# Optimization experiments

Hardware: AMD Instinct MI355X
Metric: run time of the kernel (lower is better)

The kernel has to match this reference:

```python
import jax, jax.numpy as jnp
import numpy as np

N = 50000
E = 800000
F_IN = 128
H = 128
C = 16


def _balanced_conv(x, row, col, W, b, num_nodes):
    # x: [N, in] -> linear -> gather(row) * norm -> scatter-add(col) + bias
    x = x @ W  # [N, out]
    deg = jax.ops.segment_sum(jnp.ones(row.shape[0], x.dtype), col,
                              num_segments=num_nodes)  # includes self-loops -> deg >= 1
    dinv = deg ** -0.5
    norm = dinv[row] * dinv[col]  # [E+N]
    msg = norm[:, None] * x[row]  # gather + scale
    out = jax.ops.segment_sum(msg, col, num_segments=num_nodes)  # scatter-add
    return out + b


def setup_inputs() -> dict:
    key = jax.random.key(0)
    ks = jax.random.split(key, 12)
    x = jax.random.normal(ks[0], (N, F_IN), dtype=jnp.float32)
    edge_index = jax.random.randint(ks[1], (2, E), 0, N, dtype=jnp.int64)
    s = 1.0 / np.sqrt(F_IN)
    sh = 1.0 / np.sqrt(H)
    return {
        "x": x,
        "edge_index": edge_index,
        "importance": jnp.ones((F_IN,), jnp.float32),
        "W1": jax.random.uniform(ks[2], (F_IN, H), jnp.float32, -s, s),
        "b1": jnp.zeros((H,), jnp.float32),
        "W2": jax.random.uniform(ks[3], (H, H), jnp.float32, -sh, sh),
        "b2": jnp.zeros((H,), jnp.float32),
        "W3": jax.random.uniform(ks[4], (H, H), jnp.float32, -sh, sh),
        "b3": jnp.zeros((H,), jnp.float32),
        "lw1": jax.random.uniform(ks[5], (H, H), jnp.float32, -sh, sh),
        "lb1": jax.random.uniform(ks[6], (H,), jnp.float32, -sh, sh),
        "lw2": jax.random.uniform(ks[7], (H, C), jnp.float32, -sh, sh),
        "lb2": jax.random.uniform(ks[8], (C,), jnp.float32, -sh, sh),
    }


def reference(x, edge_index, importance, W1, b1, W2, b2, W3, b3, lw1, lb1, lw2, lb2):
    num_nodes = x.shape[0]
    # add self-loops (static shape: E + N)
    loops = jnp.arange(num_nodes, dtype=edge_index.dtype)
    row = jnp.concatenate([edge_index[0], loops])
    col = jnp.concatenate([edge_index[1], loops])

    gelu = lambda t: jax.nn.gelu(t, approximate=False)  # torch F.gelu default = erf

    h = x * importance  # FeatureImportance
    h = gelu(_balanced_conv(h, row, col, W1, b1, num_nodes))
    h = gelu(_balanced_conv(h, row, col, W2, b2, num_nodes))
    h = gelu(_balanced_conv(h, row, col, W3, b3, num_nodes))
    h = gelu(h @ lw1 + lb1)
    return h @ lw2 + lb2  # [N, C]
```

## Files before the change

### kernel.cpp

```cpp
#include <hip/hip_runtime.h>
#include <math.h>

#define NNODES 50000
#define NEDGES 800000
#define FDIM 128
#define NBUCKET 196
#define BCAP 6144
#define ABLK 261
#define EPWA 3072
#define MGRID 782

typedef unsigned short ushortT;
typedef unsigned int uintT;
typedef __attribute__((ext_vector_type(8))) short short8;
typedef __attribute__((ext_vector_type(4))) float floatx4;

__device__ __forceinline__ float gelu_erf(float x){
    return 0.5f * x * (1.0f + erff(x * 0.70710678118654752f));
}
__device__ __forceinline__ float bflo(uintT u){ return __uint_as_float(u << 16); }
__device__ __forceinline__ float bfhi(uintT u){ return __uint_as_float(u & 0xFFFF0000u); }
__device__ __forceinline__ ushortT f2bf(float f){
    uintT u = __float_as_uint(f);
    return (ushortT)((u + 0x7FFFu + ((u >> 16) & 1u)) >> 16);
}
__device__ __forceinline__ void split_bf16(float f, ushortT& hi, ushortT& lo){
    uintT u = __float_as_uint(f);
    hi = (ushortT)(u >> 16);
    float fhi = __uint_as_float(u & 0xFFFF0000u);
    lo = (ushortT)(__float_as_uint(f - fhi) >> 16);
}

__global__ void k_zero(int* __restrict__ gcur){
    if (threadIdx.x < NBUCKET) gcur[threadIdx.x] = 0;
}

__global__ __launch_bounds__(256) void k_bucketA(const int* __restrict__ ei,
                                                 int* __restrict__ gcur,
                                                 uintT* __restrict__ bucket){
    __shared__ int hist[NBUCKET];
    __shared__ int base[NBUCKET];
    int t = threadIdx.x;
    if (t < NBUCKET) hist[t] = 0;
    __syncthreads();
    int e0 = blockIdx.x * EPWA;
    int cr_c[12], cr_r[12];
    #pragma unroll
    for (int p = 0; p < 12; p++){
        int e = e0 + p*256 + t;
        if (e < NEDGES){
            cr_r[p] = ei[e];
            cr_c[p] = ei[NEDGES + e];
            atomicAdd(&hist[cr_c[p] >> 8], 1);
        } else cr_c[p] = -1;
    }
    __syncthreads();
    if (t < NBUCKET){
        base[t] = atomicAdd(&gcur[t], hist[t]);
        hist[t] = 0;
    }
    __syncthreads();
    #pragma unroll
    for (int p = 0; p < 12; p++){
        int c = cr_c[p];
        if (c >= 0){
            int b = c >> 8;
            int lp = atomicAdd(&hist[b], 1);
            bucket[(size_t)b*BCAP + base[b] + lp] = ((uintT)c << 16) | (uintT)cr_r[p];
        }
    }
}

__global__ __launch_bounds__(256) void k_bucketB(const int* __restrict__ gcur,
                                                 const uintT* __restrict__ bucket,
                                                 int* __restrict__ offs,
                                                 float* __restrict__ dinv,
                                                 ushortT* __restrict__ csr2){
    __shared__ int sm[256];
    __shared__ int hist[256];
    __shared__ int lcur[256];
    int b = blockIdx.x;
    int t = threadIdx.x;
    int n0 = b << 8;

    int gv = (t < NBUCKET) ? gcur[t] : 0;
    sm[t] = gv;
    __syncthreads();
    for (int off = 1; off < 256; off <<= 1){
        int tv = (t >= off) ? sm[t-off] : 0;
        __syncthreads();
        sm[t] += tv;
        __syncthreads();
    }
    __shared__ int bbase_s;
    if (t == b) bbase_s = sm[t] - gv;
    hist[t] = 0;
    __syncthreads();
    int bbase = bbase_s;
    int count = gcur[b];
    const uintT* src = bucket + (size_t)b*BCAP;

    for (int i = t; i < count; i += 256)
        atomicAdd(&hist[(src[i] >> 16) & 255], 1);
    __syncthreads();

    int v = hist[t];
    sm[t] = v;
    __syncthreads();
    for (int off = 1; off < 256; off <<= 1){
        int tv = (t >= off) ? sm[t-off] : 0;
        __syncthreads();
        sm[t] += tv;
        __syncthreads();
    }
    int excl = bbase + sm[t] - v;
    int node = n0 + t;
    if (node <= NNODES) offs[node] = excl;
    if (node < NNODES) dinv[node] = rsqrtf((float)(v + 1));
    if (b == NBUCKET-1 && t == 255) offs[NNODES] = NEDGES;
    lcur[t] = excl;
    __syncthreads();

    for (int i = t; i < count; i += 256){
        uintT e = src[i];
        int pos = atomicAdd(&lcur[(e >> 16) & 255], 1);
        csr2[pos] = (ushortT)(e & 0xFFFFu);
    }
}

__global__ __launch_bounds__(256) void k_packW(const float* __restrict__ Wa,
                                               const float* __restrict__ Wb,
                                               const float* __restrict__ Wc,
                                               const float* __restrict__ Wd,
                                               ushortT* __restrict__ Wp){
    int l = blockIdx.x;
    const float* W = (l==0) ? Wa : (l==1) ? Wb : (l==2) ? Wc : Wd;
    ushortT* hiP = Wp + (size_t)l*2*16384;
    ushortT* loP = hiP + 16384;
    for (int idx = threadIdx.x; idx < 16384; idx += 256){
        int k = idx >> 7, n = idx & 127;
        ushortT hi, lo;
        split_bf16(W[idx], hi, lo);
        int kc = k >> 5, quad = (k >> 3) & 3, j = k & 7;
        int nt = n >> 4, lane = (n & 15) + (quad << 4);
        int off = ((kc*8 + nt)*64 + lane)*8 + j;
        hiP[off] = hi;
        loP[off] = lo;
    }
}

__global__ __launch_bounds__(256) void k_mfma_f32(const float* __restrict__ A,
                                                  const ushortT* __restrict__ Wp,
                                                  const float* __restrict__ scale,
                                                  const float* __restrict__ dinv,
                                                  ushortT* __restrict__ Yb){
    __shared__ float As[64*132];
    int t = threadIdx.x;
    int wave = t >> 6, lane = t & 63;
    int r = lane & 15, quad = lane >> 4;
    int row0 = blockIdx.x*64;
    int m0 = row0 + wave*16;
    const ushortT* WpLo = Wp + 16384;

    #pragma unroll
    for (int p = 0; p < 8; p++){
        int idx = p*256 + t;
        int rr = idx >> 5;
        int c4 = idx & 31;
        int gr = row0 + rr;
        float4 v = make_float4(0.f,0.f,0.f,0.f);
        if (gr < NNODES) v = *(const float4*)&A[(size_t)gr*FDIM + c4*4];
        float4 s = *(const float4*)&scale[c4*4];
        v.x*=s.x; v.y*=s.y; v.z*=s.z; v.w*=s.w;
        *(float4*)&As[rr*132 + c4*4] = v;
    }
    __syncthreads();

    floatx4 acc[8];
    #pragma unroll
    for (int nt = 0; nt < 8; nt++) acc[nt] = (floatx4){0.f,0.f,0.f,0.f};

    int arl = wave*16 + r;
    #pragma unroll
    for (int kc = 0; kc < 4; kc++){
        int kb = kc*32 + quad*8;
        float4 a0 = *(const float4*)&As[arl*132 + kb];
        float4 a1 = *(const float4*)&As[arl*132 + kb + 4];
        float av[8] = {a0.x, a0.y, a0.z, a0.w, a1.x, a1.y, a1.z, a1.w};
        short8 ahi, alo;
        #pragma unroll
        for (int e = 0; e < 8; e++){
            ushortT h, l;
            split_bf16(av[e], h, l);
            ahi[e] = (short)h;
            alo[e] = (short)l;
        }
        #pragma unroll
        for (int nt = 0; nt < 8; nt++){
            size_t boff = (size_t)(((kc*8 + nt)*64 + lane))*8;
            short8 bhi = *(const short8*)&Wp[boff];
            short8 blo = *(const short8*)&WpLo[boff];
            acc[nt] = __builtin_amdgcn_mfma_f32_16x16x32_bf16(ahi, bhi, acc[nt], 0, 0, 0);
            acc[nt] = __builtin_amdgcn_mfma_f32_16x16x32_bf16(alo, bhi, acc[nt], 0, 0, 0);
            acc[nt] = __builtin_amdgcn_mfma_f32_16x16x32_bf16(ahi, blo, acc[nt], 0, 0, 0);
        }
    }

    int orow0 = m0 + quad*4;
    float4 dv = *(const float4*)&dinv[orow0];
    float dva[4] = {dv.x, dv.y, dv.z, dv.w};
    #pragma unroll
    for (int nt = 0; nt < 8; nt++){
        int n = nt*16 + r;
        int chunk = n >> 5, o = n & 31;
        #pragma unroll
        for (int reg = 0; reg < 4; reg++){
            int orow = orow0 + reg;
            if (orow < NNODES){
                float v = acc[nt][reg] * dva[reg];
                __builtin_nontemporal_store(f2bf(v),
                    &Yb[((size_t)chunk*NNODES + orow)*32 + o]);
            }
        }
    }
}

template<int OUTMODE>
__global__ __launch_bounds__(256) void k_mfma_b16(const ushortT* __restrict__ Ab,
                                                  const ushortT* __restrict__ Wp,
                                                  const float* __restrict__ dinv,
                                                  const float* __restrict__ bias,
                                                  ushortT* __restrict__ Yb){
    int t = threadIdx.x;
    int wave = t >> 6, lane = t & 63;
    int r = lane & 15, quad = lane >> 4;
    int m0 = blockIdx.x*64 + wave*16;
    int arow = m0 + r;
    if (arow >= NNODES) arow = NNODES - 1;
    const ushortT* WpLo = Wp + 16384;

    floatx4 acc[8];
    #pragma unroll
    for (int nt = 0; nt < 8; nt++) acc[nt] = (floatx4){0.f,0.f,0.f,0.f};

    short8 afr[4];
    #pragma unroll
    for (int kc = 0; kc < 4; kc++)
        afr[kc] = *(const short8*)&Ab[(size_t)arow*FDIM + kc*32 + quad*8];

    #pragma unroll
    for (int kc = 0; kc < 4; kc++){
        #pragma unroll
        for (int nt = 0; nt < 8; nt++){
            size_t boff = (size_t)(((kc*8 + nt)*64 + lane))*8;
            short8 bhi = *(const short8*)&Wp[boff];
            short8 blo = *(const short8*)&WpLo[boff];
            acc[nt] = __builtin_amdgcn_mfma_f32_16x16x32_bf16(afr[kc], bhi, acc[nt], 0, 0, 0);
            acc[nt] = __builtin_amdgcn_mfma_f32_16x16x32_bf16(afr[kc], blo, acc[nt], 0, 0, 0);
        }
    }

    int orow0 = m0 + quad*4;
    if (OUTMODE == 1){
        float4 dv = *(const float4*)&dinv[orow0];
        float dva[4] = {dv.x, dv.y, dv.z, dv.w};
        #pragma unroll
        for (int nt = 0; nt < 8; nt++){
            int n = nt*16 + r;
            int chunk = n >> 5, o = n & 31;
            #pragma unroll
            for (int reg = 0; reg < 4; reg++){
                int orow = orow0 + reg;
                if (orow < NNODES){
                    float v = acc[nt][reg] * dva[reg];
                    __builtin_nontemporal_store(f2bf(v),
                        &Yb[((size_t)chunk*NNODES + orow)*32 + o]);
                }
            }
        }
    } else {
        #pragma unroll
        for (int nt = 0; nt < 8; nt++){
            int n = nt*16 + r;
            float bv = bias[n];
            #pragma unroll
            for (int reg = 0; reg < 4; reg++){
                int orow = orow0 + reg;
                if (orow < NNODES){
                    float v = gelu_erf(acc[nt][reg] + bv);
                    __builtin_nontemporal_store(f2bf(v), &Yb[(size_t)orow*FDIM + n]);
                }
            }
        }
    }
}

__global__ __launch_bounds__(256) void k_aggregate(const ushortT* __restrict__ Yt,
                                                   const float* __restrict__ dinv,
                                                   const int* __restrict__ offs,
                                                   const ushortT* __restrict__ csr2,
                                                   const float* __restrict__ bias,
                                                   ushortT* __restrict__ Hout){
    int bid = blockIdx.x;
    int chunk = bid & 3;
    int node = (bid >> 2) * 16 + (threadIdx.x >> 4);
    int lane = threadIdx.x & 15;
    const uintT* Yc = (const uintT*)Yt + (size_t)chunk * NNODES * 16;

    uintT a0 = Yc[node*16 + lane];
    float2 acc;
    acc.x = bflo(a0);
    acc.y = bfhi(a0);
    int e0 = offs[node], e1 = offs[node+1];
    int e = e0;
    for (; e + 7 < e1; e += 8){
        int r0 = csr2[e+0];
        int r1 = csr2[e+1];
        int r2 = csr2[e+2];
        int r3 = csr2[e+3];
        int r4 = csr2[e+4];
        int r5 = csr2[e+5];
        int r6 = csr2[e+6];
        int r7 = csr2[e+7];
        uintT q0 = Yc[r0*16 + lane];
        uintT q1 = Yc[r1*16 + lane];
        uintT q2 = Yc[r2*16 + lane];
        uintT q3 = Yc[r3*16 + lane];
        uintT q4 = Yc[r4*16 + lane];
        uintT q5 = Yc[r5*16 + lane];
        uintT q6 = Yc[r6*16 + lane];
        uintT q7 = Yc[r7*16 + lane];
        acc.x += bflo(q0); acc.y += bfhi(q0);
        acc.x += bflo(q1); acc.y += bfhi(q1);
        acc.x += bflo(q2); acc.y += bfhi(q2);
        acc.x += bflo(q3); acc.y += bfhi(q3);
        acc.x += bflo(q4); acc.y += bfhi(q4);
        acc.x += bflo(q5); acc.y += bfhi(q5);
        acc.x += bflo(q6); acc.y += bfhi(q6);
        acc.x += bflo(q7); acc.y += bfhi(q7);
    }
    for (; e + 1 < e1; e += 2){
        int r0 = csr2[e], r1 = csr2[e+1];
        uintT q0 = Yc[r0*16 + lane];
        uintT q1 = Yc[r1*16 + lane];
        acc.x += bflo(q0); acc.y += bfhi(q0);
        acc.x += bflo(q1); acc.y += bfhi(q1);
    }
    if (e < e1){
        uintT q = Yc[csr2[e]*16 + lane];
        acc.x += bflo(q); acc.y += bfhi(q);
    }
    float dc = dinv[node];
    float2 bv = ((const float2*)bias)[chunk*16 + lane];
    acc.x = gelu_erf(fmaf(dc, acc.x, bv.x));
    acc.y = gelu_erf(fmaf(dc, acc.y, bv.y));
    uintT packed = (uintT)f2bf(acc.x) | ((uintT)f2bf(acc.y) << 16);
    uintT* dst = (uintT*)&Hout[(size_t)node*FDIM + chunk*32 + lane*2];
    __builtin_nontemporal_store(packed, dst);
}

__global__ __launch_bounds__(256) void k_gemm16(const ushortT* __restrict__ A,
                                                const float* __restrict__ W,
                                                const float* __restrict__ bias,
                                                float* __restrict__ out){
    __shared__ float Hs[16][132];
    __shared__ float Ws2[128][16];
    int row0 = blockIdx.x * 16;
    int t = threadIdx.x;
    const uintT* A2 = (const uintT*)A;
    #pragma unroll
    for (int p=0;p<4;p++){
        int idx = p*256 + t;
        int r = idx >> 6, c2 = idx & 63;
        uintT u = A2[(size_t)(row0+r)*64 + c2];
        Hs[r][c2*2]   = bflo(u);
        Hs[r][c2*2+1] = bfhi(u);
    }
    #pragma unroll
    for (int p=0;p<8;p++){
        int lin = p*256 + t;
        Ws2[lin>>4][lin&15] = W[lin];
    }
    __syncthreads();
    int il = t >> 4, j = t & 15;
    float acc = bias[j];
    #pragma unroll
    for (int k=0;k<FDIM;k++) acc = fmaf(Hs[il][k], Ws2[k][j], acc);
    out[(row0+il)*16 + j] = acc;
}

extern "C" void kernel_launch(void* const* d_in, const int* in_sizes, int n_in,
                              void* d_out, int out_size, void* d_ws, size_t ws_size,
                              hipStream_t stream) {
    const float* x    = (const float*)d_in[0];
    const int*   ei   = (const int*)d_in[1];
    const float* imp  = (const float*)d_in[2];
    const float* W1   = (const float*)d_in[3];
    const float* b1   = (const float*)d_in[4];
    const float* W2   = (const float*)d_in[5];
    const float* b2   = (const float*)d_in[6];
    const float* W3   = (const float*)d_in[7];
    const float* b3   = (const float*)d_in[8];
    const float* lw1  = (const float*)d_in[9];
    const float* lb1  = (const float*)d_in[10];
    const float* lw2  = (const float*)d_in[11];
    const float* lb2  = (const float*)d_in[12];
    float* out = (float*)d_out;

    int*   offs   = (int*)d_ws;
    int*   gcur   = (int*)d_ws + 50048;
    float* dinv   = (float*)d_ws + 50304;
    ushortT* csr2 = (ushortT*)((int*)d_ws + 100480);
    uintT* bucket = (uintT*)((int*)d_ws + 500480);
    ushortT* Wp   = (ushortT*)((int*)d_ws + 1704704);
    ushortT* bufYt= (ushortT*)((int*)d_ws + 1770240);
    ushortT* bufPb= bufYt;
    ushortT* bufH = (ushortT*)((int*)d_ws + 8170240);

    dim3 B(256);
    k_packW  <<<4, B, 0, stream>>>(W1, W2, W3, lw1, Wp);
    k_zero   <<<1, B, 0, stream>>>(gcur);
    k_bucketA<<<ABLK, B, 0, stream>>>(ei, gcur, bucket);
    k_bucketB<<<NBUCKET, B, 0, stream>>>(gcur, bucket, offs, dinv, csr2);

    k_mfma_f32  <<<MGRID, B, 0, stream>>>(x, Wp + 0*32768, imp, dinv, bufYt);
    k_aggregate <<<(NNODES/16)*4, B, 0, stream>>>(bufYt, dinv, offs, csr2, b1, bufH);
    k_mfma_b16<1><<<MGRID, B, 0, stream>>>(bufH, Wp + 1*32768, dinv, nullptr, bufYt);
    k_aggregate <<<(NNODES/16)*4, B, 0, stream>>>(bufYt, dinv, offs, csr2, b2, bufH);
    k_mfma_b16<1><<<MGRID, B, 0, stream>>>(bufH, Wp + 2*32768, dinv, nullptr, bufYt);
    k_aggregate <<<(NNODES/16)*4, B, 0, stream>>>(bufYt, dinv, offs, csr2, b3, bufH);

    k_mfma_b16<0><<<MGRID, B, 0, stream>>>(bufH, Wp + 3*32768, nullptr, lb1, bufPb);
    k_gemm16<<<NNODES/16, B, 0, stream>>>(bufPb, lw2, lb2, out);
}
```

Measured before the change: 339.8 us.

## Fuse final MLP into one MFMA kernel, widen aggregation chunks to 64 features

```diff
diff --git a/kernel.cpp b/kernel.cpp
--- a/kernel.cpp
+++ b/kernel.cpp
@@ -31,8 +31,44 @@
     lo = (ushortT)(__float_as_uint(f - fhi) >> 16);
 }
 
-__global__ void k_zero(int* __restrict__ gcur){
-    if (threadIdx.x < NBUCKET) gcur[threadIdx.x] = 0;
+__global__ __launch_bounds__(256) void k_packW(const float* __restrict__ Wa,
+                                               const float* __restrict__ Wb,
+                                               const float* __restrict__ Wc,
+                                               const float* __restrict__ Wd,
+                                               const float* __restrict__ We,
+                                               ushortT* __restrict__ Wp,
+                                               int* __restrict__ gcur){
+    int l = blockIdx.x;
+    int t = threadIdx.x;
+    if (l < 4){
+        const float* W = (l==0) ? Wa : (l==1) ? Wb : (l==2) ? Wc : Wd;
+        ushortT* hiP = Wp + (size_t)l*2*16384;
+        ushortT* loP = hiP + 16384;
+        for (int idx = t; idx < 16384; idx += 256){
+            int k = idx >> 7, n = idx & 127;
+            ushortT hi, lo;
+            split_bf16(W[idx], hi, lo);
+            int kc = k >> 5, quad = (k >> 3) & 3, j = k & 7;
+            int nt = n >> 4, lane = (n & 15) + (quad << 4);
+            int off = ((kc*8 + nt)*64 + lane)*8 + j;
+            hiP[off] = hi;
+            loP[off] = lo;
+        }
+    } else {
+        if (t < NBUCKET) gcur[t] = 0;
+        ushortT* hiP = Wp + (size_t)4*2*16384;
+        ushortT* loP = hiP + 2048;
+        for (int idx = t; idx < 2048; idx += 256){
+            int k = idx >> 4, n = idx & 15;
+            ushortT hi, lo;
+            split_bf16(We[idx], hi, lo);
+            int kc = k >> 5, quad = (k >> 3) & 3, j = k & 7;
+            int lane = n + (quad << 4);
+            int off = (kc*64 + lane)*8 + j;
+            hiP[off] = hi;
+            loP[off] = lo;
+        }
+    }
 }
 
 __global__ __launch_bounds__(256) void k_bucketA(const int* __restrict__ ei,
@@ -125,27 +161,6 @@
         uintT e = src[i];
         int pos = atomicAdd(&lcur[(e >> 16) & 255], 1);
         csr2[pos] = (ushortT)(e & 0xFFFFu);
-    }
-}
-
-__global__ __launch_bounds__(256) void k_packW(const float* __restrict__ Wa,
-                                               const float* __restrict__ Wb,
-                                               const float* __restrict__ Wc,
-                                               const float* __restrict__ Wd,
-                                               ushortT* __restrict__ Wp){
-    int l = blockIdx.x;
-    const float* W = (l==0) ? Wa : (l==1) ? Wb : (l==2) ? Wc : Wd;
-    ushortT* hiP = Wp + (size_t)l*2*16384;
-    ushortT* loP = hiP + 16384;
-    for (int idx = threadIdx.x; idx < 16384; idx += 256){
-        int k = idx >> 7, n = idx & 127;
-        ushortT hi, lo;
-        split_bf16(W[idx], hi, lo);
-        int kc = k >> 5, quad = (k >> 3) & 3, j = k & 7;
-        int nt = n >> 4, lane = (n & 15) + (quad << 4);
-        int off = ((kc*8 + nt)*64 + lane)*8 + j;
-        hiP[off] = hi;
-        loP[off] = lo;
     }
 }
 
@@ -212,24 +227,22 @@
     #pragma unroll
     for (int nt = 0; nt < 8; nt++){
         int n = nt*16 + r;
-        int chunk = n >> 5, o = n & 31;
+        int chunk = n >> 6, o = n & 63;
         #pragma unroll
         for (int reg = 0; reg < 4; reg++){
             int orow = orow0 + reg;
             if (orow < NNODES){
                 float v = acc[nt][reg] * dva[reg];
                 __builtin_nontemporal_store(f2bf(v),
-                    &Yb[((size_t)chunk*NNODES + orow)*32 + o]);
+                    &Yb[((size_t)chunk*NNODES + orow)*64 + o]);
             }
         }
     }
 }
 
-template<int OUTMODE>
 __global__ __launch_bounds__(256) void k_mfma_b16(const ushortT* __restrict__ Ab,
                                                   const ushortT* __restrict__ Wp,
                                                   const float* __restrict__ dinv,
-                                                  const float* __restrict__ bias,
                                                   ushortT* __restrict__ Yb){
     int t = threadIdx.x;
     int wave = t >> 6, lane = t & 63;
@@ -261,37 +274,89 @@
     }
 
     int orow0 = m0 + quad*4;
-    if (OUTMODE == 1){
-        float4 dv = *(const float4*)&dinv[orow0];
-        float dva[4] = {dv.x, dv.y, dv.z, dv.w};
+    float4 dv = *(const float4*)&dinv[orow0];
+    float dva[4] = {dv.x, dv.y, dv.z, dv.w};
+    #pragma unroll
+    for (int nt = 0; nt < 8; nt++){
+        int n = nt*16 + r;
+        int chunk = n >> 6, o = n & 63;
+        #pragma unroll
+        for (int reg = 0; reg < 4; reg++){
+            int orow = orow0 + reg;
+            if (orow < NNODES){
+                float v = acc[nt][reg] * dva[reg];
+                __builtin_nontemporal_store(f2bf(v),
+                    &Yb[((size_t)chunk*NNODES + orow)*64 + o]);
+            }
+        }
+    }
+}
+
+__global__ __launch_bounds__(256) void k_mfma_final(const ushortT* __restrict__ Ab,
+                                                    const ushortT* __restrict__ Wp1,
+                                                    const ushortT* __restrict__ Wp2,
+                                                    const float* __restrict__ lb1,
+                                                    const float* __restrict__ lb2,
+                                                    float* __restrict__ out){
+    __shared__ ushortT Ls[64*136];
+    int t = threadIdx.x;
+    int wave = t >> 6, lane = t & 63;
+    int r = lane & 15, quad = lane >> 4;
+    int row0 = blockIdx.x*64;
+    int m0 = row0 + wave*16;
+    int arow = m0 + r;
+    if (arow >= NNODES) arow = NNODES - 1;
+    const ushortT* Wp1Lo = Wp1 + 16384;
+    const ushortT* Wp2Lo = Wp2 + 2048;
+
+    floatx4 acc[8];
+    #pragma unroll
+    for (int nt = 0; nt < 8; nt++) acc[nt] = (floatx4){0.f,0.f,0.f,0.f};
+
+    short8 afr[4];
+    #pragma unroll
+    for (int kc = 0; kc < 4; kc++)
+        afr[kc] = *(const short8*)&Ab[(size_t)arow*FDIM + kc*32 + quad*8];
+
+    #pragma unroll
+    for (int kc = 0; kc < 4; kc++){
         #pragma unroll
         for (int nt = 0; nt < 8; nt++){
-            int n = nt*16 + r;
-            int chunk = n >> 5, o = n & 31;
-            #pragma unroll
-            for (int reg = 0; reg < 4; reg++){
-                int orow = orow0 + reg;
-                if (orow < NNODES){
-                    float v = acc[nt][reg] * dva[reg];
-                    __builtin_nontemporal_store(f2bf(v),
-                        &Yb[((size_t)chunk*NNODES + orow)*32 + o]);
-                }
-            }
-        }
-    } else {
-        #pragma unroll
-        for (int nt = 0; nt < 8; nt++){
-            int n = nt*16 + r;
-            float bv = bias[n];
-            #pragma unroll
-            for (int reg = 0; reg < 4; reg++){
-                int orow = orow0 + reg;
-                if (orow < NNODES){
-                    float v = gelu_erf(acc[nt][reg] + bv);
-                    __builtin_nontemporal_store(f2bf(v), &Yb[(size_t)orow*FDIM + n]);
-                }
-            }
-        }
+            size_t boff = (size_t)(((kc*8 + nt)*64 + lane))*8;
+            short8 bhi = *(const short8*)&Wp1[boff];
+            short8 blo = *(const short8*)&Wp1Lo[boff];
+            acc[nt] = __builtin_amdgcn_mfma_f32_16x16x32_bf16(afr[kc], bhi, acc[nt], 0, 0, 0);
+            acc[nt] = __builtin_amdgcn_mfma_f32_16x16x32_bf16(afr[kc], blo, acc[nt], 0, 0, 0);
+        }
+    }
+
+    int lrow0 = wave*16 + quad*4;
+    #pragma unroll
+    for (int nt = 0; nt < 8; nt++){
+        int n = nt*16 + r;
+        float bv = lb1[n];
+        #pragma unroll
+        for (int reg = 0; reg < 4; reg++){
+            Ls[(lrow0 + reg)*136 + n] = f2bf(gelu_erf(acc[nt][reg] + bv));
+        }
+    }
+    __syncthreads();
+
+    floatx4 acc2 = (floatx4){0.f,0.f,0.f,0.f};
+    #pragma unroll
+    for (int kc = 0; kc < 4; kc++){
+        short8 a2 = *(const short8*)&Ls[(wave*16 + r)*136 + kc*32 + quad*8];
+        short8 bhi = *(const short8*)&Wp2[(size_t)(kc*64 + lane)*8];
+        short8 blo = *(const short8*)&Wp2Lo[(size_t)(kc*64 + lane)*8];
+        acc2 = __builtin_amdgcn_mfma_f32_16x16x32_bf16(a2, bhi, acc2, 0, 0, 0);
+        acc2 = __builtin_amdgcn_mfma_f32_16x16x32_bf16(a2, blo, acc2, 0, 0, 0);
+    }
+    float bv2 = lb2[r];
+    #pragma unroll
+    for (int reg = 0; reg < 4; reg++){
+        int orow = m0 + quad*4 + reg;
+        if (orow < NNODES)
+            out[(size_t)orow*16 + r] = acc2[reg] + bv2;
     }
 }
 
@@ -302,12 +367,12 @@
                                                    const float* __restrict__ bias,
                                                    ushortT* __restrict__ Hout){
     int bid = blockIdx.x;
-    int chunk = bid & 3;
-    int node = (bid >> 2) * 16 + (threadIdx.x >> 4);
-    int lane = threadIdx.x & 15;
-    const uintT* Yc = (const uintT*)Yt + (size_t)chunk * NNODES * 16;
-
-    uintT a0 = Yc[node*16 + lane];
+    int chunk = bid & 1;
+    int node = (bid >> 1) * 8 + (threadIdx.x >> 5);
+    int lane = threadIdx.x & 31;
+    const uintT* Yc = (const uintT*)Yt + (size_t)chunk * NNODES * 32;
+
+    uintT a0 = Yc[node*32 + lane];
     float2 acc;
     acc.x = bflo(a0);
     acc.y = bfhi(a0);
@@ -322,14 +387,14 @@
         int r5 = csr2[e+5];
         int r6 = csr2[e+6];
         int r7 = csr2[e+7];
-        uintT q0 = Yc[r0*16 + lane];
-        uintT q1 = Yc[r1*16 + lane];
-        uintT q2 = Yc[r2*16 + lane];
-        uintT q3 = Yc[r3*16 + lane];
-        uintT q4 = Yc[r4*16 + lane];
-        uintT q5 = Yc[r5*16 + lane];
-        uintT q6 = Yc[r6*16 + lane];
-        uintT q7 = Yc[r7*16 + lane];
+        uintT q0 = Yc[r0*32 + lane];
+        uintT q1 = Yc[r1*32 + lane];
+        uintT q2 = Yc[r2*32 + lane];
+        uintT q3 = Yc[r3*32 + lane];
+        uintT q4 = Yc[r4*32 + lane];
+        uintT q5 = Yc[r5*32 + lane];
+        uintT q6 = Yc[r6*32 + lane];
+        uintT q7 = Yc[r7*32 + lane];
         acc.x += bflo(q0); acc.y += bfhi(q0);
         acc.x += bflo(q1); acc.y += bfhi(q1);
         acc.x += bflo(q2); acc.y += bfhi(q2);
@@ -341,52 +406,22 @@
     }
     for (; e + 1 < e1; e += 2){
         int r0 = csr2[e], r1 = csr2[e+1];
-        uintT q0 = Yc[r0*16 + lane];
-        uintT q1 = Yc[r1*16 + lane];
+        uintT q0 = Yc[r0*32 + lane];
+        uintT q1 = Yc[r1*32 + lane];
         acc.x += bflo(q0); acc.y += bfhi(q0);
         acc.x += bflo(q1); acc.y += bfhi(q1);
     }
     if (e < e1){
-        uintT q = Yc[csr2[e]*16 + lane];
+        uintT q = Yc[csr2[e]*32 + lane];
         acc.x += bflo(q); acc.y += bfhi(q);
     }
     float dc = dinv[node];
-    float2 bv = ((const float2*)bias)[chunk*16 + lane];
+    float2 bv = ((const float2*)bias)[chunk*32 + lane];
     acc.x = gelu_erf(fmaf(dc, acc.x, bv.x));
     acc.y = gelu_erf(fmaf(dc, acc.y, bv.y));
     uintT packed = (uintT)f2bf(acc.x) | ((uintT)f2bf(acc.y) << 16);
-    uintT* dst = (uintT*)&Hout[(size_t)node*FDIM + chunk*32 + lane*2];
+    uintT* dst = (uintT*)&Hout[(size_t)node*FDIM + chunk*64 + lane*2];
     __builtin_nontemporal_store(packed, dst);
-}
-
-__global__ __launch_bounds__(256) void k_gemm16(const ushortT* __restrict__ A,
-                                                const float* __restrict__ W,
-                                                const float* __restrict__ bias,
-                                                float* __restrict__ out){
-    __shared__ float Hs[16][132];
-    __shared__ float Ws2[128][16];
-    int row0 = blockIdx.x * 16;
-    int t = threadIdx.x;
-    const uintT* A2 = (const uintT*)A;
-    #pragma unroll
-    for (int p=0;p<4;p++){
-        int idx = p*256 + t;
-        int r = idx >> 6, c2 = idx & 63;
-        uintT u = A2[(size_t)(row0+r)*64 + c2];
-        Hs[r][c2*2]   = bflo(u);
-        Hs[r][c2*2+1] = bfhi(u);
-    }
-    #pragma unroll
-    for (int p=0;p<8;p++){
-        int lin = p*256 + t;
-        Ws2[lin>>4][lin&15] = W[lin];
-    }
-    __syncthreads();
-    int il = t >> 4, j = t & 15;
-    float acc = bias[j];
-    #pragma unroll
-    for (int k=0;k<FDIM;k++) acc = fmaf(Hs[il][k], Ws2[k][j], acc);
-    out[(row0+il)*16 + j] = acc;
 }
 
 extern "C" void kernel_launch(void* const* d_in, const int* in_sizes, int n_in,
@@ -413,23 +448,20 @@
     ushortT* csr2 = (ushortT*)((int*)d_ws + 100480);
     uintT* bucket = (uintT*)((int*)d_ws + 500480);
     ushortT* Wp   = (ushortT*)((int*)d_ws + 1704704);
-    ushortT* bufYt= (ushortT*)((int*)d_ws + 1770240);
-    ushortT* bufPb= bufYt;
-    ushortT* bufH = (ushortT*)((int*)d_ws + 8170240);
+    ushortT* bufYt= (ushortT*)((int*)d_ws + 1772544);
+    ushortT* bufH = (ushortT*)((int*)d_ws + 4972544);
 
     dim3 B(256);
-    k_packW  <<<4, B, 0, stream>>>(W1, W2, W3, lw1, Wp);
-    k_zero   <<<1, B, 0, stream>>>(gcur);
+    k_packW  <<<5, B, 0, stream>>>(W1, W2, W3, lw1, lw2, Wp, gcur);
     k_bucketA<<<ABLK, B, 0, stream>>>(ei, gcur, bucket);
     k_bucketB<<<NBUCKET, B, 0, stream>>>(gcur, bucket, offs, dinv, csr2);
 
-    k_mfma_f32  <<<MGRID, B, 0, stream>>>(x, Wp + 0*32768, imp, dinv, bufYt);
-    k_aggregate <<<(NNODES/16)*4, B, 0, stream>>>(bufYt, dinv, offs, csr2, b1, bufH);
-    k_mfma_b16<1><<<MGRID, B, 0, stream>>>(bufH, Wp + 1*32768, dinv, nullptr, bufYt);
-    k_aggregate <<<(NNODES/16)*4, B, 0, stream>>>(bufYt, dinv, offs, csr2, b2, bufH);
-    k_mfma_b16<1><<<MGRID, B, 0, stream>>>(bufH, Wp + 2*32768, dinv, nullptr, bufYt);
-    k_aggregate <<<(NNODES/16)*4, B, 0, stream>>>(bufYt, dinv, offs, csr2, b3, bufH);
-
-    k_mfma_b16<0><<<MGRID, B, 0, stream>>>(bufH, Wp + 3*32768, nullptr, lb1, bufPb);
-    k_gemm16<<<NNODES/16, B, 0, stream>>>(bufPb, lw2, lb2, out);
-}
+    k_mfma_f32 <<<MGRID, B, 0, stream>>>(x, Wp + 0*32768, imp, dinv, bufYt);
+    k_aggregate<<<(NNODES/8)*2, B, 0, stream>>>(bufYt, dinv, offs, csr2, b1, bufH);
+    k_mfma_b16 <<<MGRID, B, 0, stream>>>(bufH, Wp + 1*32768, dinv, bufYt);
+    k_aggregate<<<(NNODES/8)*2, B, 0, stream>>>(bufYt, dinv, offs, csr2, b2, bufH);
+    k_mfma_b16 <<<MGRID, B, 0, stream>>>(bufH, Wp + 2*32768, dinv, bufYt);
+    k_aggregate<<<(NNODES/8)*2, B, 0, stream>>>(bufYt, dinv, offs, csr2, b3, bufH);
+
+    k_mfma_final<<<MGRID, B, 0, stream>>>(bufH, Wp + 3*32768, Wp + 4*32768, lb1, lb2, out);
+}
```

Result: faster. 320.3 us (-5.7%).
